# Performance work log

Hardware: AMD Instinct MI355X
Metric: run time of the kernel (lower is better)

## Reference

```python
import jax, jax.numpy as jnp
import numpy as np


def setup_inputs() -> dict:
    key = jax.random.key(0)
    k1, k2 = jax.random.split(key)
    B, F, L, K = 8, 64, 131072, 9
    x = jax.random.normal(k1, (B, F, L), dtype=jnp.float32)
    # Xavier-uniform-like init for kernel (F, 1, K)
    limit = float(np.sqrt(6.0 / (1 * K + F * K)))
    kernel = jax.random.uniform(k2, (F, 1, K), dtype=jnp.float32, minval=-limit, maxval=limit)
    return {"x": x, "kernel": kernel}


def reference(x, kernel):
    # x: (B, F, L); kernel: (F, 1, K). Original loops over F filters, convolving
    # channel i of x with kernel[i] (stride=1, padding='same', bias=0), which is a
    # depthwise grouped conv. Original stacks results as (F, B, 1, L).
    B, F, L = x.shape
    out = jax.lax.conv_general_dilated(
        x, kernel,
        window_strides=(1,),
        padding='SAME',  # stride 1, matches torch 'same' (left=floor, right=ceil)
        feature_group_count=F,
        dimension_numbers=('NCH', 'OIH', 'NCH'),
    )  # (B, F, L)
    return jnp.transpose(out, (1, 0, 2))[:, :, None, :]  # (F, B, 1, L)
```

## Files before the change

### kernel.cpp

```cpp
#include <hip/hip_runtime.h>


#define BB 8
#define FF 64
#define LL 131072
#define KK 9
#define CHUNK 1024
#define CPR (LL / CHUNK)
#define CPR_SHIFT 7
#define NROWS (BB * FF)
#define LDS_N (CHUNK + 8)

__global__ __launch_bounds__(256) void dwconv1d_kernel(
    const float* __restrict__ x,
    const float* __restrict__ kern,
    float* __restrict__ out)
{
    __shared__ float s[LDS_N];

    const int c       = blockIdx.x;
    const int chunk   = c & (CPR - 1);
    const int row_out = c >> CPR_SHIFT;
    const int f       = row_out >> 3;
    const int b       = row_out & 7;

    const float* xrow = x + ((size_t)(b * FF + f)) * (size_t)LL;
    const int l0 = chunk << 10;
    const int t  = threadIdx.x;

    #pragma unroll
    for (int v = t; v < LDS_N / 4; v += 256) {
        const int g = l0 - 4 + 4 * v;
        float4 val = make_float4(0.f, 0.f, 0.f, 0.f);
        if (g >= 0 && g + 3 < LL) val = *(const float4*)(xrow + g);
        *(float4*)(&s[4 * v]) = val;
    }

    float w[KK];
    #pragma unroll
    for (int k = 0; k < KK; ++k) w[k] = kern[f * KK + k];

    __syncthreads();

    float xin[12];
    #pragma unroll
    for (int m = 0; m < 12; ++m) xin[m] = s[4 * t + m];

    float acc[4];
    #pragma unroll
    for (int j = 0; j < 4; ++j) {
        float v0 = 0.f;
        #pragma unroll
        for (int k = 0; k < KK; ++k) v0 += w[k] * xin[j + k];
        acc[j] = v0;
    }

    float4 o = make_float4(acc[0], acc[1], acc[2], acc[3]);
    *(float4*)(out + (size_t)row_out * (size_t)LL + l0 + 4 * t) = o;
}

extern "C" void kernel_launch(void* const* d_in, const int* in_sizes, int n_in,
                              void* d_out, int out_size, void* d_ws, size_t ws_size,
                              hipStream_t stream) {
    const float* x    = (const float*)d_in[0];
    const float* kern = (const float*)d_in[1];
    float* out        = (float*)d_out;

    const int grid  = NROWS * CPR;
    const int block = 256;

    hipLaunchKernelGGL(dwconv1d_kernel, dim3(grid), dim3(block), 0, stream,
                       x, kern, out);
}
```

Measured before the change: 438.4 us.

## Replace LDS staging with direct overlapping global float4 loads, two quads per thread

```diff
diff --git a/kernel.cpp b/kernel.cpp
--- a/kernel.cpp
+++ b/kernel.cpp
@@ -5,58 +5,73 @@
 #define FF 64
 #define LL 131072
 #define KK 9
-#define CHUNK 1024
+#define CHUNK 2048
 #define CPR (LL / CHUNK)
-#define CPR_SHIFT 7
+#define CPR_SHIFT 6
 #define NROWS (BB * FF)
-#define LDS_N (CHUNK + 8)
+#define QPT 2
 
 __global__ __launch_bounds__(256) void dwconv1d_kernel(
     const float* __restrict__ x,
     const float* __restrict__ kern,
     float* __restrict__ out)
 {
-    __shared__ float s[LDS_N];
-
     const int c       = blockIdx.x;
     const int chunk   = c & (CPR - 1);
     const int row_out = c >> CPR_SHIFT;
     const int f       = row_out >> 3;
     const int b       = row_out & 7;
 
-    const float* xrow = x + ((size_t)(b * FF + f)) * (size_t)LL;
-    const int l0 = chunk << 10;
-    const int t  = threadIdx.x;
+    const float* __restrict__ xrow = x + ((size_t)(b * FF + f)) * (size_t)LL;
+    float* __restrict__ orow       = out + (size_t)row_out * (size_t)LL;
 
-    #pragma unroll
-    for (int v = t; v < LDS_N / 4; v += 256) {
-        const int g = l0 - 4 + 4 * v;
-        float4 val = make_float4(0.f, 0.f, 0.f, 0.f);
-        if (g >= 0 && g + 3 < LL) val = *(const float4*)(xrow + g);
-        *(float4*)(&s[4 * v]) = val;
-    }
+    const int l0    = chunk << 11;
+    const int t     = threadIdx.x;
+    const int base0 = l0 + 4 * t;
 
     float w[KK];
     #pragma unroll
     for (int k = 0; k < KK; ++k) w[k] = kern[f * KK + k];
 
-    __syncthreads();
+    float4 va[QPT], vb[QPT], vc[QPT];
 
-    float xin[12];
-    #pragma unroll
-    for (int m = 0; m < 12; ++m) xin[m] = s[4 * t + m];
-
-    float acc[4];
-    #pragma unroll
-    for (int j = 0; j < 4; ++j) {
-        float v0 = 0.f;
+    if (chunk != 0 && chunk != CPR - 1) {
         #pragma unroll
-        for (int k = 0; k < KK; ++k) v0 += w[k] * xin[j + k];
-        acc[j] = v0;
+        for (int q = 0; q < QPT; ++q) {
+            const float* p = xrow + base0 + 1024 * q;
+            va[q] = *(const float4*)(p - 4);
+            vb[q] = *(const float4*)(p);
+            vc[q] = *(const float4*)(p + 4);
+        }
+    } else {
+        #pragma unroll
+        for (int q = 0; q < QPT; ++q) {
+            const int l    = base0 + 1024 * q;
+            const float* p = xrow + l;
+            va[q] = (l - 4 >= 0) ? *(const float4*)(p - 4)
+                                 : make_float4(0.f, 0.f, 0.f, 0.f);
+            vb[q] = *(const float4*)(p);
+            vc[q] = (l + 7 < LL) ? *(const float4*)(p + 4)
+                                 : make_float4(0.f, 0.f, 0.f, 0.f);
+        }
     }
 
-    float4 o = make_float4(acc[0], acc[1], acc[2], acc[3]);
-    *(float4*)(out + (size_t)row_out * (size_t)LL + l0 + 4 * t) = o;
+    #pragma unroll
+    for (int q = 0; q < QPT; ++q) {
+        const float xin[12] = { va[q].x, va[q].y, va[q].z, va[q].w,
+                                vb[q].x, vb[q].y, vb[q].z, vb[q].w,
+                                vc[q].x, vc[q].y, vc[q].z, vc[q].w };
+        float acc[4];
+        #pragma unroll
+        for (int j = 0; j < 4; ++j) {
+            float v0 = 0.f;
+            #pragma unroll
+            for (int k = 0; k < KK; ++k) v0 += w[k] * xin[j + k];
+            acc[j] = v0;
+        }
+        *(float4*)(orow + base0 + 1024 * q) =
+            make_float4(acc[0], acc[1], acc[2], acc[3]);
+    }
 }
 
 extern "C" void kernel_launch(void* const* d_in, const int* in_sizes, int n_in,
```

After: 445.0 us. No clear change (+1.5%).

## Use persistent blocks with register-prefetched overlapping loads and nontemporal stores

Applied to the files above, without the earlier changes.

```diff
diff --git a/kernel.cpp b/kernel.cpp
--- a/kernel.cpp
+++ b/kernel.cpp
@@ -7,56 +7,82 @@
 #define KK 9
 #define CHUNK 1024
 #define CPR (LL / CHUNK)
-#define CPR_SHIFT 7
 #define NROWS (BB * FF)
-#define LDS_N (CHUNK + 8)
+#define BPR 4
+#define GRID (NROWS * BPR)
+#define ITERS (CPR / BPR)
+#define STRIDE (BPR * CHUNK)
+
+typedef float __attribute__((ext_vector_type(4))) floatx4;
+
+__device__ __forceinline__ void load_trio(const float* __restrict__ xrow,
+                                          int l0, int t,
+                                          float4& A, float4& B, float4& C)
+{
+    const int base  = l0 + 4 * t;
+    const float* p  = xrow + base;
+    if (l0 == 0 || l0 == (CPR - 1) * CHUNK) {
+        A = (base - 4 >= 0) ? *(const float4*)(p - 4)
+                            : make_float4(0.f, 0.f, 0.f, 0.f);
+        B = *(const float4*)(p);
+        C = (base + 7 < LL) ? *(const float4*)(p + 4)
+                            : make_float4(0.f, 0.f, 0.f, 0.f);
+    } else {
+        A = *(const float4*)(p - 4);
+        B = *(const float4*)(p);
+        C = *(const float4*)(p + 4);
+    }
+}
 
 __global__ __launch_bounds__(256) void dwconv1d_kernel(
     const float* __restrict__ x,
     const float* __restrict__ kern,
     float* __restrict__ out)
 {
-    __shared__ float s[LDS_N];
-
-    const int c       = blockIdx.x;
-    const int chunk   = c & (CPR - 1);
-    const int row_out = c >> CPR_SHIFT;
+    const int n       = blockIdx.x;
+    const int row_out = n >> 2;
+    const int sub     = n & (BPR - 1);
     const int f       = row_out >> 3;
     const int b       = row_out & 7;
 
-    const float* xrow = x + ((size_t)(b * FF + f)) * (size_t)LL;
-    const int l0 = chunk << 10;
-    const int t  = threadIdx.x;
+    const float* __restrict__ xrow = x + ((size_t)(b * FF + f)) * (size_t)LL;
+    float* __restrict__ orow       = out + (size_t)row_out * (size_t)LL;
 
-    #pragma unroll
-    for (int v = t; v < LDS_N / 4; v += 256) {
-        const int g = l0 - 4 + 4 * v;
-        float4 val = make_float4(0.f, 0.f, 0.f, 0.f);
-        if (g >= 0 && g + 3 < LL) val = *(const float4*)(xrow + g);
-        *(float4*)(&s[4 * v]) = val;
-    }
+    const int t = threadIdx.x;
 
     float w[KK];
     #pragma unroll
     for (int k = 0; k < KK; ++k) w[k] = kern[f * KK + k];
 
-    __syncthreads();
+    int l0 = sub * CHUNK;
 
-    float xin[12];
-    #pragma unroll
-    for (int m = 0; m < 12; ++m) xin[m] = s[4 * t + m];
+    float4 a0, b0, c0;
+    load_trio(xrow, l0, t, a0, b0, c0);
 
-    float acc[4];
-    #pragma unroll
-    for (int j = 0; j < 4; ++j) {
-        float v0 = 0.f;
+    #pragma unroll 4
+    for (int i = 0; i < ITERS; ++i) {
+        const int l0n = l0 + STRIDE;
+
+        float4 a1, b1, c1;
+        if (i + 1 < ITERS) load_trio(xrow, l0n, t, a1, b1, c1);
+
+        const float xin[12] = { a0.x, a0.y, a0.z, a0.w,
+                                b0.x, b0.y, b0.z, b0.w,
+                                c0.x, c0.y, c0.z, c0.w };
+        float acc[4];
         #pragma unroll
-        for (int k = 0; k < KK; ++k) v0 += w[k] * xin[j + k];
-        acc[j] = v0;
+        for (int j = 0; j < 4; ++j) {
+            float v0 = 0.f;
+            #pragma unroll
+            for (int k = 0; k < KK; ++k) v0 += w[k] * xin[j + k];
+            acc[j] = v0;
+        }
+        floatx4 o = { acc[0], acc[1], acc[2], acc[3] };
+        __builtin_nontemporal_store(o, (floatx4*)(orow + l0 + 4 * t));
+
+        a0 = a1; b0 = b1; c0 = c1;
+        l0 = l0n;
     }
-
-    float4 o = make_float4(acc[0], acc[1], acc[2], acc[3]);
-    *(float4*)(out + (size_t)row_out * (size_t)LL + l0 + 4 * t) = o;
 }
 
 extern "C" void kernel_launch(void* const* d_in, const int* in_sizes, int n_in,
@@ -66,9 +92,6 @@
     const float* kern = (const float*)d_in[1];
     float* out        = (float*)d_out;
 
-    const int grid  = NROWS * CPR;
-    const int block = 256;
-
-    hipLaunchKernelGGL(dwconv1d_kernel, dim3(grid), dim3(block), 0, stream,
+    hipLaunchKernelGGL(dwconv1d_kernel, dim3(GRID), dim3(256), 0, stream,
                        x, kern, out);
 }
```

New measurement: 460.0 us. 4.9% more time.
